# Performance work log

Hardware: AMD Instinct MI355X
Metric: run time of the kernel (lower is better)

The kernel has to match this reference:

```python
import jax, jax.numpy as jnp
import numpy as np

B, T, L = 1024, 1024, 32
START_ID, STOP_ID = 0, 1
NEG_INF = -10000.0


def setup_inputs() -> dict:
    key = jax.random.key(0)
    k1, k2, k3 = jax.random.split(key, 3)
    features = jax.random.normal(k1, (B, T, L), dtype=jnp.float32)
    label_ids = jax.random.randint(k2, (B, T), 0, L)
    transitions = jax.random.normal(k3, (L, L), dtype=jnp.float32)
    # replicate the init-time masking of start row / stop column
    transitions = transitions.at[START_ID, :].set(NEG_INF)
    transitions = transitions.at[:, STOP_ID].set(NEG_INF)
    return {"features": features, "transitions": transitions, "label_ids": label_ids}


def reference(features, transitions, label_ids):
    # training-mode forward: neg log likelihood = mean(logZ - gold_score)
    b, t, l = features.shape

    # --- forward (alpha) recursion over time via scan ---
    alpha0 = jnp.full((b, l), NEG_INF, dtype=features.dtype).at[:, START_ID].set(0.0)
    feats_tm = jnp.swapaxes(features, 0, 1)[1:]  # [T-1, B, L], time-major

    def step(alpha, feat_t):
        # new_alpha[b, i] = lse_j(transitions[i, j] + alpha[b, j]) + feat_t[b, i]
        new_alpha = jax.nn.logsumexp(transitions[None, :, :] + alpha[:, None, :], axis=-1) + feat_t
        return new_alpha, None

    alpha_T, _ = jax.lax.scan(step, alpha0, feats_tm)
    forward_score = jax.nn.logsumexp(alpha_T, axis=-1)  # [B], log partition

    # --- gold path score, vectorized over time ---
    cur, prev = label_ids[:, 1:], label_ids[:, :-1]          # [B, T-1]
    trans_score = transitions[cur, prev]                      # [B, T-1]
    emit_score = jnp.take_along_axis(features[:, 1:], cur[:, :, None], axis=-1)[..., 0]
    gold_score = jnp.sum(trans_score + emit_score, axis=-1)   # [B]

    return jnp.mean(forward_score - gold_score)
```

## Files before the change

kernel.cpp:

```cpp
#include <hip/hip_runtime.h>
#include <hip/hip_bf16.h>


constexpr int BN = 1024, TN = 1024, LN = 32;
constexpr float KSHIFT = 8.5f;
constexpr float LN2F   = 0.69314718056f;

typedef __attribute__((ext_vector_type(8)))  short bf16x8;
typedef __attribute__((ext_vector_type(16))) float f32x16;
typedef __attribute__((ext_vector_type(2)))  float f32x2;

static __device__ __forceinline__ unsigned pktrunc(float a, float b) {
    return __builtin_amdgcn_perm(__float_as_uint(b), __float_as_uint(a), 0x07060302u);
}
#define PLSWAP(a, b) asm("v_permlane32_swap_b32 %0, %1" : "+v"(a), "+v"(b))

__global__ __launch_bounds__(256, 4) void crf_chunk(
    const float* __restrict__ feat,
    const float* __restrict__ trans,
    const int*   __restrict__ lab,
    float* __restrict__ ws,
    float* __restrict__ out,
    int CHS)
{
    const int CH = 1 << CHS, LEN = TN >> CHS;
    const int l = threadIdx.x & 63, n = l & 31, h = l >> 5;
    const int wid = __builtin_amdgcn_readfirstlane((int)(threadIdx.x >> 6));
    const int gid = blockIdx.x * 4 + wid;
    const int c = gid & (CH - 1), b = gid >> CHS;

    const float* __restrict__ fb = feat + (size_t)b * TN * LN;
    const int*   __restrict__ lb = lab  + (size_t)b * TN;

    f32x2 EA[4], EB[4];
    #pragma unroll
    for (int r = 0; r < 4; ++r) {
        EA[r][0] = __expf(trans[n * LN + 8 * h + 2 * r]          - KSHIFT);
        EA[r][1] = __expf(trans[n * LN + 8 * h + 2 * r + 1]      - KSHIFT);
        EB[r][0] = __expf(trans[n * LN + 16 + 8 * h + 2 * r]     - KSHIFT);
        EB[r][1] = __expf(trans[n * LN + 16 + 8 * h + 2 * r + 1] - KSHIFT);
    }

    union BU { bf16x8 v; unsigned u[4]; } B1f, B2f;
    #pragma unroll
    for (int r = 0; r < 4; ++r) {
        int k0 = 8 * h + 2 * r, k1 = k0 + 1;
        B1f.u[r] = (k0 == n ? 0x3F80u : 0u) | ((k1 == n ? 0x3F80u : 0u) << 16);
        B2f.u[r] = (k0 + 16 == n ? 0x3F80u : 0u) | ((k1 + 16 == n ? 0x3F80u : 0u) << 16);
    }

    const int start = c * LEN, te = start + LEN;
    const int tm = (c == 0) ? 2 : start;

    float gold = 0.f;
    int pv;
    if (c == 0) {
        int c0 = lb[1];
        gold = trans[c0 * LN + lb[0]] + fb[LN + c0];
        pv = c0;
    } else {
        pv = lb[start - 1];
    }
    int   ct = lb[tm];
    int   c1 = lb[tm + 1];
    float gt = trans[ct * LN + pv];
    float gf = fb[(size_t)tm * LN + ct];

    float fcur = fb[(size_t)tm * LN + n];
    float f1   = fb[(size_t)(tm + 1) * LN + n];

    int sc = 0;
    f32x16 ZR;
    #pragma unroll
    for (int i = 0; i < 16; ++i) ZR[i] = 0.f;
    f32x16 C;

    for (int t = tm; t < te; ++t) {
        const int tp2 = (t + 2 < te) ? (t + 2) : (te - 1);
        const int tp1 = (t + 1 < te) ? (t + 1) : (te - 1);
        float f2 = fb[(size_t)tp2 * LN + n];
        int   c2 = lb[tp2];

        gold += gt + gf;
        float gtn = trans[c1 * LN + ct];
        float gfn = fb[(size_t)tp1 * LN + c1];

        float F = __expf(fcur);
        f32x2 F2; F2[0] = F; F2[1] = F;
        union BU A1, A2;
        #pragma unroll
        for (int r = 0; r < 4; ++r) {
            f32x2 pa = EA[r] * F2;
            f32x2 pb = EB[r] * F2;
            A1.u[r] = pktrunc(pa[0], pa[1]);
            A2.u[r] = pktrunc(pb[0], pb[1]);
        }

        C = __builtin_amdgcn_mfma_f32_32x32x16_bf16(A1.v, B1f.v, ZR, 0, 0, 0);
        C = __builtin_amdgcn_mfma_f32_32x32x16_bf16(A2.v, B2f.v, C, 0, 0, 0);

        if ((t & 15) == 15) {
            float cm = C[0];
            #pragma unroll
            for (int i = 1; i < 16; ++i) cm = fmaxf(cm, C[i]);
            unsigned ca = __float_as_uint(cm), cb = ca;
            PLSWAP(ca, cb);
            cm = fmaxf(__uint_as_float(ca), __uint_as_float(cb));
            cm = fmaxf(cm, 1e-30f);
            int ex; frexpf(cm, &ex);
            sc += ex;
            #pragma unroll
            for (int i = 0; i < 16; ++i) C[i] = ldexpf(C[i], -ex);
        }

        unsigned PK[8];
        #pragma unroll
        for (int r = 0; r < 8; ++r) PK[r] = pktrunc(C[2 * r], C[2 * r + 1]);
        PLSWAP(PK[0], PK[2]);  PLSWAP(PK[1], PK[3]);
        PLSWAP(PK[4], PK[6]);  PLSWAP(PK[5], PK[7]);
        B1f.u[0] = PK[0]; B1f.u[1] = PK[1]; B1f.u[2] = PK[2]; B1f.u[3] = PK[3];
        B2f.u[0] = PK[4]; B2f.u[1] = PK[5]; B2f.u[2] = PK[6]; B2f.u[3] = PK[7];

        fcur = f1; f1 = f2;
        gt = gtn; gf = gfn;
        ct = c1;  c1 = c2;
    }

    if (l == 0) atomicAdd(out, -gold * (1.0f / (float)BN));

    const float add = KSHIFT * (float)(te - tm) + (float)sc * LN2F;
    float* __restrict__ w = ws + ((size_t)gid << 10);
    #pragma unroll
    for (int r = 0; r < 16; ++r) {
        int row = (r & 3) + 8 * (r >> 2) + 4 * h;
        float v = C[r];
        w[row * LN + n] = (v > 0.f) ? (__logf(v) + add) : -10000.0f;
    }
}

__global__ __launch_bounds__(64) void crf_combine(
    const float* __restrict__ trans,
    const float* __restrict__ feat,
    const float* __restrict__ ws,
    float* __restrict__ out,
    int CHS)
{
    const int CH = 1 << CHS;
    const int l = threadIdx.x & 63, i = l & 31;
    const int seq = blockIdx.x * 2 + (l >> 5);
    const int bb = (l & 32) << 2;

    float alpha = trans[i * LN] + feat[(size_t)seq * TN * LN + LN + i];
    const float* __restrict__ wsb = ws + ((size_t)seq << (10 + CHS));

    for (int c = 0; c < CH; ++c) {
        const float4* Mr = (const float4*)(wsb + (c << 10) + i * LN);
        float vv[32];
        #pragma unroll
        for (int q = 0; q < 8; ++q) {
            float4 m4 = Mr[q];
            vv[4 * q + 0] = m4.x; vv[4 * q + 1] = m4.y;
            vv[4 * q + 2] = m4.z; vv[4 * q + 3] = m4.w;
        }
        float mx = -1e30f;
        #pragma unroll
        for (int j = 0; j < 32; ++j) {
            int r = __builtin_amdgcn_ds_bpermute(bb + (j << 2), __float_as_int(alpha));
            vv[j] += __int_as_float(r);
            mx = fmaxf(mx, vv[j]);
        }
        float s = 0.f;
        #pragma unroll
        for (int j = 0; j < 32; ++j) s += __expf(vv[j] - mx);
        alpha = mx + __logf(s);
    }

    float m = alpha;
    #pragma unroll
    for (int s = 16; s; s >>= 1) m = fmaxf(m, __shfl_xor(m, s, 32));
    float es = __expf(alpha - m);
    #pragma unroll
    for (int s = 16; s; s >>= 1) es += __shfl_xor(es, s, 32);
    float fs = m + __logf(es);

    if (i == 0) atomicAdd(out, fs * (1.0f / (float)BN));
}

extern "C" void kernel_launch(void* const* d_in, const int* in_sizes, int n_in,
                              void* d_out, int out_size, void* d_ws, size_t ws_size,
                              hipStream_t stream) {
    const float* features    = (const float*)d_in[0];
    const float* transitions = (const float*)d_in[1];
    const int*   labels      = (const int*)d_in[2];
    float* out = (float*)d_out;
    float* ws  = (float*)d_ws;

    int CHS = 3;
    while (CHS > 0 && ws_size < (((size_t)BN << CHS) * (LN * LN * 4))) --CHS;
    const int CH = 1 << CHS;

    hipMemsetAsync(out, 0, sizeof(float), stream);
    crf_chunk<<<dim3((BN * CH) / 4), dim3(256), 0, stream>>>(
        features, transitions, labels, ws, out, CHS);
    crf_combine<<<dim3(BN / 2), dim3(64), 0, stream>>>(
        transitions, features, ws, out, CHS);
}
```

Measured before the change: 210.8 us.

## Hoist gold-path scoring out of recurrence and software-pipeline A-matrix construction

Gold path score is now computed up front by each wave with lanes striding over time and a wave-wide shuffle reduction, which removes the per-step dependent label/transition gathers from the serial recurrence loop. The recurrence loop builds the next step's A operands (exp of features times exp transitions) while the current MFMAs run, and prefetches features four steps ahead with an unroll of 2. This shortens the loop-carried critical path at the cost of extra registers for the double-buffered operands.

```diff
diff --git a/kernel.cpp b/kernel.cpp
--- a/kernel.cpp
+++ b/kernel.cpp
@@ -32,6 +32,24 @@
     const float* __restrict__ fb = feat + (size_t)b * TN * LN;
     const int*   __restrict__ lb = lab  + (size_t)b * TN;
 
+    const int start = c * LEN, te = start + LEN;
+    const int tm = (c == 0) ? 2 : start;
+
+    {
+        float gsum = 0.f;
+        for (int r = 0; r < LEN; r += 64) {
+            int t = start + r + l;
+            if (t >= 1) {
+                int cur = lb[t];
+                int prv = lb[t - 1];
+                gsum += trans[cur * LN + prv] + fb[(size_t)t * LN + cur];
+            }
+        }
+        #pragma unroll
+        for (int s = 32; s; s >>= 1) gsum += __shfl_xor(gsum, s, 64);
+        if (l == 0) atomicAdd(out, -gsum * (1.0f / (float)BN));
+    }
+
     f32x2 EA[4], EB[4];
     #pragma unroll
     for (int r = 0; r < 4; ++r) {
@@ -49,45 +67,15 @@
         B2f.u[r] = (k0 + 16 == n ? 0x3F80u : 0u) | ((k1 + 16 == n ? 0x3F80u : 0u) << 16);
     }
 
-    const int start = c * LEN, te = start + LEN;
-    const int tm = (c == 0) ? 2 : start;
-
-    float gold = 0.f;
-    int pv;
-    if (c == 0) {
-        int c0 = lb[1];
-        gold = trans[c0 * LN + lb[0]] + fb[LN + c0];
-        pv = c0;
-    } else {
-        pv = lb[start - 1];
-    }
-    int   ct = lb[tm];
-    int   c1 = lb[tm + 1];
-    float gt = trans[ct * LN + pv];
-    float gf = fb[(size_t)tm * LN + ct];
-
     float fcur = fb[(size_t)tm * LN + n];
     float f1   = fb[(size_t)(tm + 1) * LN + n];
-
-    int sc = 0;
-    f32x16 ZR;
-    #pragma unroll
-    for (int i = 0; i < 16; ++i) ZR[i] = 0.f;
-    f32x16 C;
-
-    for (int t = tm; t < te; ++t) {
-        const int tp2 = (t + 2 < te) ? (t + 2) : (te - 1);
-        const int tp1 = (t + 1 < te) ? (t + 1) : (te - 1);
-        float f2 = fb[(size_t)tp2 * LN + n];
-        int   c2 = lb[tp2];
-
-        gold += gt + gf;
-        float gtn = trans[c1 * LN + ct];
-        float gfn = fb[(size_t)tp1 * LN + c1];
-
+    float f2   = fb[(size_t)(tm + 2) * LN + n];
+    float f3   = fb[(size_t)(tm + 3) * LN + n];
+
+    union BU A1, A2, A1n, A2n;
+    {
         float F = __expf(fcur);
         f32x2 F2; F2[0] = F; F2[1] = F;
-        union BU A1, A2;
         #pragma unroll
         for (int r = 0; r < 4; ++r) {
             f32x2 pa = EA[r] * F2;
@@ -95,9 +83,31 @@
             A1.u[r] = pktrunc(pa[0], pa[1]);
             A2.u[r] = pktrunc(pb[0], pb[1]);
         }
-
+    }
+
+    int sc = 0;
+    f32x16 ZR;
+    #pragma unroll
+    for (int i = 0; i < 16; ++i) ZR[i] = 0.f;
+    f32x16 C;
+
+    #pragma unroll 2
+    for (int t = tm; t < te; ++t) {
         C = __builtin_amdgcn_mfma_f32_32x32x16_bf16(A1.v, B1f.v, ZR, 0, 0, 0);
         C = __builtin_amdgcn_mfma_f32_32x32x16_bf16(A2.v, B2f.v, C, 0, 0, 0);
+
+        const int tp = (t + 4 < te) ? (t + 4) : (te - 1);
+        float fl = fb[(size_t)tp * LN + n];
+
+        float F = __expf(f1);
+        f32x2 F2; F2[0] = F; F2[1] = F;
+        #pragma unroll
+        for (int r = 0; r < 4; ++r) {
+            f32x2 pa = EA[r] * F2;
+            f32x2 pb = EB[r] * F2;
+            A1n.u[r] = pktrunc(pa[0], pa[1]);
+            A2n.u[r] = pktrunc(pb[0], pb[1]);
+        }
 
         if ((t & 15) == 15) {
             float cm = C[0];
@@ -121,12 +131,9 @@
         B1f.u[0] = PK[0]; B1f.u[1] = PK[1]; B1f.u[2] = PK[2]; B1f.u[3] = PK[3];
         B2f.u[0] = PK[4]; B2f.u[1] = PK[5]; B2f.u[2] = PK[6]; B2f.u[3] = PK[7];
 
-        fcur = f1; f1 = f2;
-        gt = gtn; gf = gfn;
-        ct = c1;  c1 = c2;
-    }
-
-    if (l == 0) atomicAdd(out, -gold * (1.0f / (float)BN));
+        A1 = A1n; A2 = A2n;
+        f1 = f2; f2 = f3; f3 = fl;
+    }
 
     const float add = KSHIFT * (float)(te - tm) + (float)sc * LN2F;
     float* __restrict__ w = ws + ((size_t)gid << 10);
```

Measured after the change: 247.7 us. +17.5%, slower.
